# Kernel optimization log

Measured on AMD Instinct MI355X. Metric: run time of the kernel, lower is better.

## Reference

```python
import jax, jax.numpy as jnp
import numpy as np

ALPHA = 0.044194173824159216  # 1/sqrt(512)
EPS = 1e-6
C, G, HW = 512, 32, 4096


def setup_inputs() -> dict:
    key = jax.random.key(0)
    ks = jax.random.split(key, 10)
    s = 1.0 / np.sqrt(C)
    return {
        "x": jax.random.normal(ks[0], (8, C, 64, 64), dtype=jnp.float32),
        "gamma": jnp.ones((C,), jnp.float32),
        "beta": jnp.zeros((C,), jnp.float32),
        "wq": jax.random.uniform(ks[1], (C, C), jnp.float32, -s, s),
        "bq": jax.random.uniform(ks[2], (C,), jnp.float32, -s, s),
        "wk": jax.random.uniform(ks[3], (C, C), jnp.float32, -s, s),
        "bk": jax.random.uniform(ks[4], (C,), jnp.float32, -s, s),
        "wv": jax.random.uniform(ks[5], (C, C), jnp.float32, -s, s),
        "bv": jax.random.uniform(ks[6], (C,), jnp.float32, -s, s),
        "wo": jax.random.uniform(ks[7], (C, C), jnp.float32, -s, s),
        "bo": jax.random.uniform(ks[8], (C,), jnp.float32, -s, s),
    }


def _group_norm(x, gamma, beta):
    B = x.shape[0]
    xg = x.reshape(B, G, C // G, 64, 64)
    mu = jnp.mean(xg, axis=(2, 3, 4), keepdims=True)
    var = jnp.var(xg, axis=(2, 3, 4), keepdims=True)
    xn = ((xg - mu) / jnp.sqrt(var + EPS)).reshape(B, C, 64, 64)
    return xn * gamma[None, :, None, None] + beta[None, :, None, None]


def reference(x, gamma, beta, wq, bq, wk, bk, wv, bv, wo, bo):
    B = x.shape[0]
    res = x
    h = _group_norm(x, gamma, beta)
    # [B, HW, C]
    h = h.reshape(B, C, HW).transpose(0, 2, 1)
    q = h @ wq.T + bq
    k = h @ wk.T + bk
    v = h @ wv.T + bv
    # scores [B, HW, HW]
    scores = ALPHA * jnp.einsum("bnc,bmc->bnm", q, k)
    attn = jax.nn.softmax(scores, axis=2)
    o = jnp.einsum("bnm,bmc->bnc", attn, v)
    o = o @ wo.T + bo
    o = o.transpose(0, 2, 1).reshape(B, C, 64, 64)
    return o + res
```

## Files before the change

kernel.cpp:

```cpp
#include <hip/hip_runtime.h>
#include <hip/hip_bf16.h>

typedef __attribute__((ext_vector_type(8))) short short8;
typedef __attribute__((ext_vector_type(4))) float f32x4;

#define ALPHA 0.044194173824159216f

#define GLO(p) (const __attribute__((address_space(1))) void*)(p)
#define LDSP(p) (__attribute__((address_space(3))) void*)(p)

__device__ __forceinline__ unsigned short f2bf(float f) {
    union { float f; unsigned int u; } c; c.f = f;
    unsigned int u = c.u;
    return (unsigned short)((u + 0x7FFFu + ((u >> 16) & 1u)) >> 16);
}

__device__ __forceinline__ float bf2f(unsigned short s) {
    union { unsigned int u; float f; } c; c.u = ((unsigned int)s) << 16;
    return c.f;
}

__global__ __launch_bounds__(256) void gn_stats(const float* __restrict__ x,
                                                float* __restrict__ stats) {
    int blk = blockIdx.x;
    const float4* src = (const float4*)(x + (size_t)blk * 65536);
    float s = 0.f, sq = 0.f;
    for (int i = threadIdx.x; i < 16384; i += 256) {
        float4 v = src[i];
        s  += v.x + v.y + v.z + v.w;
        sq += v.x*v.x + v.y*v.y + v.z*v.z + v.w*v.w;
    }
    for (int off = 32; off; off >>= 1) {
        s  += __shfl_down(s, off);
        sq += __shfl_down(sq, off);
    }
    __shared__ float ss[4], ssq[4];
    int wid = threadIdx.x >> 6;
    if ((threadIdx.x & 63) == 0) { ss[wid] = s; ssq[wid] = sq; }
    __syncthreads();
    if (threadIdx.x == 0) {
        float S = ss[0]+ss[1]+ss[2]+ss[3], Q = ssq[0]+ssq[1]+ssq[2]+ssq[3];
        float mu = S * (1.f/65536.f);
        float var = Q * (1.f/65536.f) - mu*mu;
        stats[blk] = mu;
        stats[256 + blk] = rsqrtf(var + 1e-6f);
    }
}

__global__ __launch_bounds__(256) void wcvt(const float* __restrict__ s,
                                            unsigned short* __restrict__ d) {
    int i = blockIdx.x * 1024 + threadIdx.x * 4;
    float4 v = *(const float4*)(s + i);
    ushort4 o = make_ushort4(f2bf(v.x), f2bf(v.y), f2bf(v.z), f2bf(v.w));
    *(ushort4*)(d + i) = o;
}

__global__ __launch_bounds__(256) void zero_l(float* __restrict__ l) {
    ((float4*)l)[blockIdx.x * 256 + threadIdx.x] = make_float4(0.f, 0.f, 0.f, 0.f);
}

__global__ __launch_bounds__(256) void recip(float* __restrict__ l) {
    int i = blockIdx.x * 256 + threadIdx.x;
    float4 v = ((const float4*)l)[i];
    ((float4*)l)[i] = make_float4(1.f / v.x, 1.f / v.y, 1.f / v.z, 1.f / v.w);
}

__global__ __launch_bounds__(256) void gn_apply(const float* __restrict__ x,
                                                const float* __restrict__ stats,
                                                const float* __restrict__ gamma,
                                                const float* __restrict__ beta,
                                                unsigned short* __restrict__ h) {
    __shared__ unsigned short t[64][72];
    int b = blockIdx.z, c0 = blockIdx.y * 64, hw0 = blockIdx.x * 64;
    int tid = threadIdx.x;
#pragma unroll
    for (int rep = 0; rep < 4; ++rep) {
        int lin = rep * 256 + tid;
        int row = lin >> 4;
        int c4  = lin & 15;
        int c   = c0 + row;
        const float4* src = (const float4*)(x + ((size_t)(b*512 + c) << 12) + hw0);
        float4 v = src[c4];
        int sidx = b*32 + (c >> 4);
        float mu = stats[sidx], rs = stats[256 + sidx];
        float ga = gamma[c] * rs, be = beta[c] - mu * ga;
        t[c4*4+0][row] = f2bf(v.x * ga + be);
        t[c4*4+1][row] = f2bf(v.y * ga + be);
        t[c4*4+2][row] = f2bf(v.z * ga + be);
        t[c4*4+3][row] = f2bf(v.w * ga + be);
    }
    __syncthreads();
#pragma unroll
    for (int rep = 0; rep < 2; ++rep) {
        int lin = rep * 256 + tid;
        int row = lin >> 3;
        int u8  = lin & 7;
        unsigned short* dst = h + (((size_t)(b*4096 + hw0 + row)) << 9) + c0 + u8*8;
        *(short8*)dst = *(const short8*)&t[row][u8*8];
    }
}

__global__ __launch_bounds__(256, 2) void gemm_bt(const unsigned short* __restrict__ A,
                                                  int lda, long aZs,
                                                  const unsigned short* __restrict__ B,
                                                  int ldb, long bZs,
                                                  const float* __restrict__ bias,
                                                  const float* __restrict__ resid,
                                                  const float* __restrict__ lvec,
                                                  void* __restrict__ out,
                                                  long ldo, long oZs,
                                                  int K, int mode, float scale) {
    __shared__ unsigned short As[128][72], Bs[128][72];
    int z = blockIdx.z;
    A += (size_t)z * aZs;
    B += (size_t)z * bZs;
    unsigned short* outu = (unsigned short*)out + (size_t)z * oZs;
    int m0 = blockIdx.y * 128, n0 = blockIdx.x * 128;
    int tid = threadIdx.x, w = tid >> 6, l = tid & 63;
    int lr = l & 15, lq = l >> 4, lk = lq * 8;
    int rbase = (w >> 1) * 64, cbase = (w & 1) * 64;
    f32x4 acc[4][4] = {};
    for (int k0 = 0; k0 < K; k0 += 64) {
        __syncthreads();
#pragma unroll
        for (int p = 0; p < 4; ++p) {
            int lin = p * 256 + tid;
            int r = lin >> 3, qq = lin & 7;
            *(short8*)&As[r][qq*8] = *(const short8*)(A + (size_t)(m0 + r)*lda + k0 + qq*8);
            *(short8*)&Bs[r][qq*8] = *(const short8*)(B + (size_t)(n0 + r)*ldb + k0 + qq*8);
        }
        __syncthreads();
        short8 af[4][2], bfv[4][2];
#pragma unroll
        for (int i = 0; i < 4; ++i)
#pragma unroll
            for (int ks = 0; ks < 2; ++ks) {
                af[i][ks]  = *(const short8*)&As[rbase + i*16 + lr][ks*32 + lk];
                bfv[i][ks] = *(const short8*)&Bs[cbase + i*16 + lr][ks*32 + lk];
            }
#pragma unroll
        for (int ks = 0; ks < 2; ++ks)
#pragma unroll
            for (int i = 0; i < 4; ++i)
#pragma unroll
                for (int j = 0; j < 4; ++j)
                    acc[i][j] = __builtin_amdgcn_mfma_f32_16x16x32_bf16(af[i][ks], bfv[j][ks], acc[i][j], 0, 0, 0);
    }
    int lq4 = lq * 4;
    if (mode == 2) {
        float rlv[4];
#pragma unroll
        for (int j = 0; j < 4; ++j) rlv[j] = lvec[n0 + cbase + j*16 + lr];
        float* outf = (float*)out;
#pragma unroll
        for (int i = 0; i < 4; ++i) {
            int rowg = m0 + rbase + i*16 + lq4;
            float4 bq4 = *(const float4*)(bias + rowg);
            float bb[4] = {bq4.x, bq4.y, bq4.z, bq4.w};
            size_t ad[16];
            float lres[16];
#pragma unroll
            for (int j = 0; j < 4; ++j) {
                int colg = n0 + cbase + j*16 + lr;
                size_t base = ((size_t)(colg >> 12)) * 2097152 + (size_t)(colg & 4095);
#pragma unroll
                for (int r = 0; r < 4; ++r) {
                    ad[j*4+r] = base + (size_t)(rowg + r) * 4096;
                    lres[j*4+r] = resid[ad[j*4+r]];
                }
            }
#pragma unroll
            for (int j = 0; j < 4; ++j)
#pragma unroll
                for (int r = 0; r < 4; ++r)
                    outf[ad[j*4+r]] = acc[i][j][r] * rlv[j] + bb[r] + lres[j*4+r];
        }
        return;
    }
#pragma unroll
    for (int i = 0; i < 4; ++i) {
        int rowg = m0 + rbase + i*16 + lq4;
#pragma unroll
        for (int j = 0; j < 4; ++j) {
            int colg = n0 + cbase + j*16 + lr;
#pragma unroll
            for (int r = 0; r < 4; ++r) {
                float v = acc[i][j][r];
                int rr = rowg + r;
                if (mode == 0) {
                    outu[(size_t)rr * ldo + colg] = f2bf((v + bias[colg]) * scale);
                } else {
                    outu[(size_t)rr * ldo + colg] = f2bf(v + bias[rr]);
                }
            }
        }
    }
}

__global__ __launch_bounds__(256, 2) void qk2(const unsigned short* __restrict__ A,
                                              const unsigned short* __restrict__ Wq,
                                              const unsigned short* __restrict__ Wk,
                                              const float* __restrict__ biasq,
                                              const float* __restrict__ biask,
                                              unsigned short* __restrict__ qo,
                                              unsigned short* __restrict__ ko) {
    __shared__ unsigned short As[128][72], Bq[128][72], Bk[128][72];
    int m0 = blockIdx.y * 128, n0 = blockIdx.x * 128;
    int tid = threadIdx.x, w = tid >> 6, l = tid & 63;
    int lr = l & 15, lq = l >> 4, lk = lq * 8;
    int rbase = (w >> 1) * 64, cbase = (w & 1) * 64;
    f32x4 aq[4][4] = {}, ak[4][4] = {};
    for (int k0 = 0; k0 < 512; k0 += 64) {
        __syncthreads();
#pragma unroll
        for (int p = 0; p < 4; ++p) {
            int lin = p * 256 + tid;
            int r = lin >> 3, qq = lin & 7;
            *(short8*)&As[r][qq*8] = *(const short8*)(A  + (size_t)(m0 + r)*512 + k0 + qq*8);
            *(short8*)&Bq[r][qq*8] = *(const short8*)(Wq + (size_t)(n0 + r)*512 + k0 + qq*8);
            *(short8*)&Bk[r][qq*8] = *(const short8*)(Wk + (size_t)(n0 + r)*512 + k0 + qq*8);
        }
        __syncthreads();
#pragma unroll
        for (int ks = 0; ks < 2; ++ks) {
            short8 af[4], bfq[4], bfk[4];
#pragma unroll
            for (int i = 0; i < 4; ++i) {
                af[i]  = *(const short8*)&As[rbase + i*16 + lr][ks*32 + lk];
                bfq[i] = *(const short8*)&Bq[cbase + i*16 + lr][ks*32 + lk];
                bfk[i] = *(const short8*)&Bk[cbase + i*16 + lr][ks*32 + lk];
            }
#pragma unroll
            for (int i = 0; i < 4; ++i)
#pragma unroll
                for (int j = 0; j < 4; ++j) {
                    aq[i][j] = __builtin_amdgcn_mfma_f32_16x16x32_bf16(af[i], bfq[j], aq[i][j], 0, 0, 0);
                    ak[i][j] = __builtin_amdgcn_mfma_f32_16x16x32_bf16(af[i], bfk[j], ak[i][j], 0, 0, 0);
                }
        }
    }
    int lq4 = lq * 4;
#pragma unroll
    for (int i = 0; i < 4; ++i) {
        int rowg = m0 + rbase + i*16 + lq4;
#pragma unroll
        for (int j = 0; j < 4; ++j) {
            int colg = n0 + cbase + j*16 + lr;
            float bqv = biasq[colg], bkv = biask[colg];
#pragma unroll
            for (int r = 0; r < 4; ++r) {
                qo[(size_t)(rowg + r) * 512 + colg] = f2bf((aq[i][j][r] + bqv) * ALPHA);
                ko[(size_t)(rowg + r) * 512 + colg] = f2bf(ak[i][j][r] + bkv);
            }
        }
    }
}

__device__ __forceinline__ void mm8_core(const unsigned short* __restrict__ A, int lda,
                                         const unsigned short* __restrict__ B, int ldb,
                                         int T,
                                         unsigned short (*As)[256][64],
                                         unsigned short (*Bs)[256][64],
                                         f32x4 acc[8][4]) {
    int tid = threadIdx.x, w = tid >> 6, l = tid & 63;
    int wr = w >> 2, wc = w & 3;
    int lr = l & 15, lq = l >> 4;
    int rsub = l >> 3, colp = ((l & 7) ^ rsub) << 3;
    int sw = (lr & 7) << 4;
    int aw = w * 8;

#define SG_A(buf, t_) { \
    const unsigned short* ap = A + (size_t)(t_) * 64; \
    __builtin_amdgcn_global_load_lds(GLO(ap + (size_t)(aw + rsub) * lda + colp),        LDSP(&As[buf][aw][0]), 16, 0, 0); \
    __builtin_amdgcn_global_load_lds(GLO(ap + (size_t)(64 + aw + rsub) * lda + colp),   LDSP(&As[buf][64 + aw][0]), 16, 0, 0); \
    __builtin_amdgcn_global_load_lds(GLO(ap + (size_t)(128 + aw + rsub) * lda + colp),  LDSP(&As[buf][128 + aw][0]), 16, 0, 0); \
    __builtin_amdgcn_global_load_lds(GLO(ap + (size_t)(192 + aw + rsub) * lda + colp),  LDSP(&As[buf][192 + aw][0]), 16, 0, 0); }
#define SG_B(buf, t_, h_) { \
    const unsigned short* bp = B + (size_t)(t_) * 64; int rb = (h_) * 128 + aw; \
    __builtin_amdgcn_global_load_lds(GLO(bp + (size_t)(rb + rsub) * ldb + colp),       LDSP(&Bs[buf][rb][0]), 16, 0, 0); \
    __builtin_amdgcn_global_load_lds(GLO(bp + (size_t)(rb + 64 + rsub) * ldb + colp),  LDSP(&Bs[buf][rb + 64][0]), 16, 0, 0); }
#define RD_B() { \
    const char* bsb = (const char*)Bs[cur]; \
    _Pragma("unroll") for (int nj = 0; nj < 4; ++nj) \
    _Pragma("unroll") for (int ks = 0; ks < 2; ++ks) { \
        int row = wc * 64 + nj * 16 + lr; \
        bf[nj][ks] = *(const short8*)(bsb + (((row << 7) + (ks << 6) + (lq << 4)) ^ sw)); } }
#define RD_A(p_) { \
    const char* asb = (const char*)As[cur]; \
    _Pragma("unroll") for (int i = 0; i < 2; ++i) \
    _Pragma("unroll") for (int ks = 0; ks < 2; ++ks) { \
        int row = wr * 128 + ((p_) * 2 + i) * 16 + lr; \
        af[i][ks] = *(const short8*)(asb + (((row << 7) + (ks << 6) + (lq << 4)) ^ sw)); } }
#define MM(p_) { \
    _Pragma("unroll") for (int ks = 0; ks < 2; ++ks) \
    _Pragma("unroll") for (int i = 0; i < 2; ++i) \
    _Pragma("unroll") for (int nj = 0; nj < 4; ++nj) \
        acc[(p_) * 2 + i][nj] = __builtin_amdgcn_mfma_f32_16x16x32_bf16(af[i][ks], bf[nj][ks], acc[(p_) * 2 + i][nj], 0, 0, 0); }
#define LGKM0 { asm volatile("s_waitcnt lgkmcnt(0)" ::: "memory"); __builtin_amdgcn_sched_barrier(0); }
#define VMC4 { asm volatile("s_waitcnt vmcnt(4)" ::: "memory"); __builtin_amdgcn_sched_barrier(0); }
#define VMC0 { asm volatile("s_waitcnt vmcnt(0)" ::: "memory"); __builtin_amdgcn_sched_barrier(0); }
#define BAR __builtin_amdgcn_s_barrier()

    SG_A(0, 0); SG_B(0, 0, 0); SG_B(0, 0, 1);
    if (T > 1) { SG_B(1, 1, 0); SG_B(1, 1, 1); VMC4; } else { VMC0; }
    BAR;
    for (int t = 0; t < T; ++t) {
        int cur = t & 1, nxt = cur ^ 1;
        short8 bf[4][2], af[2][2];
        RD_B(); RD_A(0);
        if (t + 1 < T) SG_A(nxt, t + 1);
        BAR; LGKM0;
        __builtin_amdgcn_s_setprio(1); MM(0); __builtin_amdgcn_s_setprio(0);
        BAR;
        RD_A(1);
        if (t + 2 < T) SG_B(cur, t + 2, 0);
        BAR; LGKM0;
        __builtin_amdgcn_s_setprio(1); MM(1); __builtin_amdgcn_s_setprio(0);
        BAR;
        RD_A(2);
        if (t + 2 < T) SG_B(cur, t + 2, 1);
        BAR; LGKM0;
        __builtin_amdgcn_s_setprio(1); MM(2); __builtin_amdgcn_s_setprio(0);
        BAR;
        RD_A(3);
        if (t + 2 < T) { VMC4; } else { VMC0; }
        BAR; LGKM0;
        __builtin_amdgcn_s_setprio(1); MM(3); __builtin_amdgcn_s_setprio(0);
        BAR;
    }
#undef SG_A
#undef SG_B
#undef RD_B
#undef RD_A
#undef MM
#undef LGKM0
#undef VMC4
#undef VMC0
#undef BAR
}

__global__ __launch_bounds__(512, 2) void s8(const unsigned short* __restrict__ q,
                                             const unsigned short* __restrict__ k,
                                             float* __restrict__ lout,
                                             unsigned short* __restrict__ P0,
                                             unsigned short* __restrict__ P1,
                                             int nwg) {
    __shared__ unsigned short As[2][256][64], Bs[2][256][64];
    int wk = (int)(blockIdx.x & 7) * (nwg >> 3) + (int)(blockIdx.x >> 3);
    int z = wk >> 8, rem = wk & 255;
    int m0 = (rem >> 4) << 8, n0 = (rem & 15) << 8;
    const unsigned short* A = k + (size_t)z * 2097152 + (size_t)m0 * 512;
    const unsigned short* B = q + (size_t)z * 2097152 + (size_t)n0 * 512;
    f32x4 acc[8][4] = {};
    mm8_core(A, 512, B, 512, 8, As, Bs, acc);
    unsigned short* Pz = (z < 2) ? P0 + (size_t)z * 16777216
                                 : P1 + (size_t)(z - 2) * 16777216;
    float* lz = lout + z * 4096;
    int tid = threadIdx.x, w = tid >> 6, l = tid & 63;
    int wr = w >> 2, wc = w & 3, lr = l & 15, lq = l >> 4, lq4 = lq * 4;
    int jb = m0 + wr * 128;
    int ib = n0 + wc * 64;
#pragma unroll
    for (int nj = 0; nj < 4; ++nj) {
        int i = ib + nj * 16 + lr;
        unsigned short* prow = Pz + (size_t)i * 4096 + jb + lq4;
        float rs = 0.f;
#pragma unroll
        for (int mi = 0; mi < 8; ++mi) {
            float e0 = __expf(acc[mi][nj][0]);
            float e1 = __expf(acc[mi][nj][1]);
            float e2 = __expf(acc[mi][nj][2]);
            float e3 = __expf(acc[mi][nj][3]);
            rs += (e0 + e1) + (e2 + e3);
            ushort4 pk = make_ushort4(f2bf(e0), f2bf(e1), f2bf(e2), f2bf(e3));
            *(ushort4*)(prow + mi * 16) = pk;
        }
        rs += __shfl_xor(rs, 16);
        rs += __shfl_xor(rs, 32);
        if (lq == 0) atomicAdd(&lz[i], rs);
    }
}

__global__ __launch_bounds__(512, 2) void pv8(const unsigned short* __restrict__ P0,
                                              const unsigned short* __restrict__ P1,
                                              const unsigned short* __restrict__ vt,
                                              unsigned short* __restrict__ part0,
                                              unsigned short* __restrict__ part1,
                                              int zofs, int nwg) {
    __shared__ unsigned short As[2][256][64], Bs[2][256][64];
    int wk = (int)(blockIdx.x & 7) * (nwg >> 3) + (int)(blockIdx.x >> 3);
    int half = nwg >> 1;
    int s = (wk >= half) ? 1 : 0;
    int rem = wk - s * half;
    int z = rem >> 5, t2 = rem & 31;
    int m0 = (t2 >> 1) << 8, n0 = (t2 & 1) << 8;
    const unsigned short* Pz = (z < 2) ? P0 + (size_t)z * 16777216
                                       : P1 + (size_t)(z - 2) * 16777216;
    const unsigned short* A = Pz + (size_t)m0 * 4096 + (size_t)s * 2048;
    const unsigned short* B = vt + (size_t)n0 * 32768 + (size_t)(zofs + z) * 4096 + (size_t)s * 2048;
    f32x4 acc[8][4] = {};
    mm8_core(A, 4096, B, 32768, 32, As, Bs, acc);
    unsigned short* pp = (s ? part1 : part0) + (size_t)z * 2097152 + (size_t)m0 * 512 + n0;
    int tid = threadIdx.x, w = tid >> 6, l = tid & 63;
    int wr = w >> 2, wc = w & 3, lr = l & 15, lq4 = (l >> 4) * 4;
#pragma unroll
    for (int mi = 0; mi < 8; ++mi)
#pragma unroll
        for (int nj = 0; nj < 4; ++nj)
#pragma unroll
            for (int r = 0; r < 4; ++r)
                pp[(size_t)(wr * 128 + mi * 16 + lq4 + r) * 512 + wc * 64 + nj * 16 + lr] = f2bf(acc[mi][nj][r]);
}

__global__ __launch_bounds__(256) void addcvt(const unsigned short* __restrict__ p0,
                                              const unsigned short* __restrict__ p1,
                                              unsigned short* __restrict__ o) {
    size_t i = ((size_t)blockIdx.x * 256 + threadIdx.x) * 8;
    short8 a = *(const short8*)(p0 + i), b = *(const short8*)(p1 + i);
    short8 r;
#pragma unroll
    for (int j = 0; j < 8; ++j)
        r[j] = (short)f2bf(bf2f((unsigned short)a[j]) + bf2f((unsigned short)b[j]));
    *(short8*)(o + i) = r;
}

extern "C" void kernel_launch(void* const* d_in, const int* in_sizes, int n_in,
                              void* d_out, int out_size, void* d_ws, size_t ws_size,
                              hipStream_t stream) {
    const float* x     = (const float*)d_in[0];
    const float* gamma = (const float*)d_in[1];
    const float* beta  = (const float*)d_in[2];
    const float* wq = (const float*)d_in[3];  const float* bq = (const float*)d_in[4];
    const float* wk = (const float*)d_in[5];  const float* bk = (const float*)d_in[6];
    const float* wv = (const float*)d_in[7];  const float* bv = (const float*)d_in[8];
    const float* wo = (const float*)d_in[9];  const float* bo = (const float*)d_in[10];

    char* wsp = (char*)d_ws;
    float* stats        = (float*)wsp;
    unsigned short* wqb = (unsigned short*)(wsp + 2048);
    unsigned short* wkb = wqb + 262144;
    unsigned short* wvb = wkb + 262144;
    unsigned short* wob = wvb + 262144;
    unsigned short* h   = wob + 262144;
    unsigned short* qb  = h  + 16777216;
    unsigned short* kb  = qb + 16777216;
    unsigned short* vtb = kb + 16777216;
    float* lbuf         = (float*)(vtb + 16777216);
    unsigned short* Pw  = (unsigned short*)(lbuf + 32768);
    unsigned short* Pd  = (unsigned short*)d_out;
    unsigned short* ob  = h;

    const bool mid = ws_size >= 204000000ull;

    gn_stats<<<256, 256, 0, stream>>>(x, stats);
    wcvt<<<256, 256, 0, stream>>>(wq, wqb);
    wcvt<<<256, 256, 0, stream>>>(wk, wkb);
    wcvt<<<256, 256, 0, stream>>>(wv, wvb);
    wcvt<<<256, 256, 0, stream>>>(wo, wob);
    gn_apply<<<dim3(64, 8, 8), 256, 0, stream>>>(x, stats, gamma, beta, h);
    zero_l<<<32, 256, 0, stream>>>(lbuf);

    qk2<<<dim3(4, 256), 256, 0, stream>>>(h, wqb, wkb, bq, bk, qb, kb);
    gemm_bt<<<dim3(256, 4), 256, 0, stream>>>(wvb, 512, 0, h, 512, 0, bv, nullptr, nullptr,
                                              vtb, 32768, 0, 512, 1, 1.0f);

    const long QS = (long)4096 * 512;
    if (mid) {
        for (int c = 0; c < 2; ++c) {
            size_t z0 = (size_t)c * 4;
            s8<<<1024, 512, 0, stream>>>(qb + z0 * QS, kb + z0 * QS,
                                         lbuf + z0 * 4096, Pd, Pw, 1024);
            pv8<<<256, 512, 0, stream>>>(Pd, Pw, vtb,
                                         qb + z0 * QS, kb + z0 * QS, (int)z0, 256);
            addcvt<<<4096, 256, 0, stream>>>(qb + z0 * QS, kb + z0 * QS, ob + z0 * QS);
        }
    } else {
        for (int c = 0; c < 4; ++c) {
            size_t z0 = (size_t)c * 2;
            s8<<<512, 512, 0, stream>>>(qb + z0 * QS, kb + z0 * QS,
                                        lbuf + z0 * 4096, Pd, Pd, 512);
            pv8<<<128, 512, 0, stream>>>(Pd, Pd, vtb,
                                         qb + z0 * QS, kb + z0 * QS, (int)z0, 128);
            addcvt<<<2048, 256, 0, stream>>>(qb + z0 * QS, kb + z0 * QS, ob + z0 * QS);
        }
    }
    recip<<<32, 256, 0, stream>>>(lbuf);
    gemm_bt<<<dim3(256, 4), 256, 0, stream>>>(wob, 512, 0, ob, 512, 0, bo, x, lbuf,
                                              d_out, 0, 0, 512, 2, 1.0f);
}
```

Before: 681.5 us.

## Fuse split-K partial add into output GEMM and replace atomics with partial sums

Removes the addcvt pass that summed the two split-K halves of the attention output, and instead has the output-projection GEMM accumulate over both partial buffers in two K passes. Row-sum atomics in s8 are replaced by per-block LDS reductions written to a partial buffer in the freed h region, and the recip kernel sums those partials. This drops the zero_l launch and a full read/write pass over the attention output, but doubles the K loop in the final GEMM and adds a 16-way partial reduction.

New measurement: 674.3 us. About the same (-1.1%).

```diff
diff --git a/kernel.cpp b/kernel.cpp
--- a/kernel.cpp
+++ b/kernel.cpp
@@ -55,14 +55,16 @@
     *(ushort4*)(d + i) = o;
 }
 
-__global__ __launch_bounds__(256) void zero_l(float* __restrict__ l) {
-    ((float4*)l)[blockIdx.x * 256 + threadIdx.x] = make_float4(0.f, 0.f, 0.f, 0.f);
-}
-
-__global__ __launch_bounds__(256) void recip(float* __restrict__ l) {
+__global__ __launch_bounds__(256) void recip(const float* __restrict__ lpart,
+                                             float* __restrict__ l) {
     int i = blockIdx.x * 256 + threadIdx.x;
-    float4 v = ((const float4*)l)[i];
-    ((float4*)l)[i] = make_float4(1.f / v.x, 1.f / v.y, 1.f / v.z, 1.f / v.w);
+    float4 s = make_float4(0.f, 0.f, 0.f, 0.f);
+#pragma unroll
+    for (int jt = 0; jt < 16; ++jt) {
+        float4 v = ((const float4*)(lpart + (size_t)jt * 32768))[i];
+        s.x += v.x; s.y += v.y; s.z += v.z; s.w += v.w;
+    }
+    ((float4*)l)[i] = make_float4(1.f/s.x, 1.f/s.y, 1.f/s.z, 1.f/s.w);
 }
 
 __global__ __launch_bounds__(256) void gn_apply(const float* __restrict__ x,
@@ -104,6 +106,7 @@
                                                   int lda, long aZs,
                                                   const unsigned short* __restrict__ B,
                                                   int ldb, long bZs,
+                                                  const unsigned short* __restrict__ B2,
                                                   const float* __restrict__ bias,
                                                   const float* __restrict__ resid,
                                                   const float* __restrict__ lvec,
@@ -120,31 +123,36 @@
     int lr = l & 15, lq = l >> 4, lk = lq * 8;
     int rbase = (w >> 1) * 64, cbase = (w & 1) * 64;
     f32x4 acc[4][4] = {};
-    for (int k0 = 0; k0 < K; k0 += 64) {
-        __syncthreads();
-#pragma unroll
-        for (int p = 0; p < 4; ++p) {
-            int lin = p * 256 + tid;
-            int r = lin >> 3, qq = lin & 7;
-            *(short8*)&As[r][qq*8] = *(const short8*)(A + (size_t)(m0 + r)*lda + k0 + qq*8);
-            *(short8*)&Bs[r][qq*8] = *(const short8*)(B + (size_t)(n0 + r)*ldb + k0 + qq*8);
-        }
-        __syncthreads();
-        short8 af[4][2], bfv[4][2];
-#pragma unroll
-        for (int i = 0; i < 4; ++i)
-#pragma unroll
-            for (int ks = 0; ks < 2; ++ks) {
-                af[i][ks]  = *(const short8*)&As[rbase + i*16 + lr][ks*32 + lk];
-                bfv[i][ks] = *(const short8*)&Bs[cbase + i*16 + lr][ks*32 + lk];
+    int passes = (mode == 2) ? 2 : 1;
+    const unsigned short* Bsrc = B;
+    for (int ps = 0; ps < passes; ++ps) {
+        if (ps) Bsrc = B2;
+        for (int k0 = 0; k0 < K; k0 += 64) {
+            __syncthreads();
+#pragma unroll
+            for (int p = 0; p < 4; ++p) {
+                int lin = p * 256 + tid;
+                int r = lin >> 3, qq = lin & 7;
+                *(short8*)&As[r][qq*8] = *(const short8*)(A + (size_t)(m0 + r)*lda + k0 + qq*8);
+                *(short8*)&Bs[r][qq*8] = *(const short8*)(Bsrc + (size_t)(n0 + r)*ldb + k0 + qq*8);
             }
-#pragma unroll
-        for (int ks = 0; ks < 2; ++ks)
+            __syncthreads();
+            short8 af[4][2], bfv[4][2];
 #pragma unroll
             for (int i = 0; i < 4; ++i)
 #pragma unroll
-                for (int j = 0; j < 4; ++j)
-                    acc[i][j] = __builtin_amdgcn_mfma_f32_16x16x32_bf16(af[i][ks], bfv[j][ks], acc[i][j], 0, 0, 0);
+                for (int ks = 0; ks < 2; ++ks) {
+                    af[i][ks]  = *(const short8*)&As[rbase + i*16 + lr][ks*32 + lk];
+                    bfv[i][ks] = *(const short8*)&Bs[cbase + i*16 + lr][ks*32 + lk];
+                }
+#pragma unroll
+            for (int ks = 0; ks < 2; ++ks)
+#pragma unroll
+                for (int i = 0; i < 4; ++i)
+#pragma unroll
+                    for (int j = 0; j < 4; ++j)
+                        acc[i][j] = __builtin_amdgcn_mfma_f32_16x16x32_bf16(af[i][ks], bfv[j][ks], acc[i][j], 0, 0, 0);
+        }
     }
     int lq4 = lq * 4;
     if (mode == 2) {
@@ -184,15 +192,8 @@
         for (int j = 0; j < 4; ++j) {
             int colg = n0 + cbase + j*16 + lr;
 #pragma unroll
-            for (int r = 0; r < 4; ++r) {
-                float v = acc[i][j][r];
-                int rr = rowg + r;
-                if (mode == 0) {
-                    outu[(size_t)rr * ldo + colg] = f2bf((v + bias[colg]) * scale);
-                } else {
-                    outu[(size_t)rr * ldo + colg] = f2bf(v + bias[rr]);
-                }
-            }
+            for (int r = 0; r < 4; ++r)
+                outu[(size_t)(rowg + r) * ldo + colg] = f2bf(acc[i][j][r] + bias[rowg + r]);
         }
     }
 }
@@ -341,10 +342,10 @@
 
 __global__ __launch_bounds__(512, 2) void s8(const unsigned short* __restrict__ q,
                                              const unsigned short* __restrict__ k,
-                                             float* __restrict__ lout,
+                                             float* __restrict__ lpart,
                                              unsigned short* __restrict__ P0,
                                              unsigned short* __restrict__ P1,
-                                             int nwg) {
+                                             int zofs, int nwg) {
     __shared__ unsigned short As[2][256][64], Bs[2][256][64];
     int wk = (int)(blockIdx.x & 7) * (nwg >> 3) + (int)(blockIdx.x >> 3);
     int z = wk >> 8, rem = wk & 255;
@@ -355,15 +356,14 @@
     mm8_core(A, 512, B, 512, 8, As, Bs, acc);
     unsigned short* Pz = (z < 2) ? P0 + (size_t)z * 16777216
                                  : P1 + (size_t)(z - 2) * 16777216;
-    float* lz = lout + z * 4096;
     int tid = threadIdx.x, w = tid >> 6, l = tid & 63;
     int wr = w >> 2, wc = w & 3, lr = l & 15, lq = l >> 4, lq4 = lq * 4;
     int jb = m0 + wr * 128;
-    int ib = n0 + wc * 64;
+    float* lsum = (float*)As;
 #pragma unroll
     for (int nj = 0; nj < 4; ++nj) {
-        int i = ib + nj * 16 + lr;
-        unsigned short* prow = Pz + (size_t)i * 4096 + jb + lq4;
+        int iloc = wc * 64 + nj * 16 + lr;
+        unsigned short* prow = Pz + (size_t)(n0 + iloc) * 4096 + jb + lq4;
         float rs = 0.f;
 #pragma unroll
         for (int mi = 0; mi < 8; ++mi) {
@@ -377,7 +377,12 @@
         }
         rs += __shfl_xor(rs, 16);
         rs += __shfl_xor(rs, 32);
-        if (lq == 0) atomicAdd(&lz[i], rs);
+        if (lq == 0) lsum[wr * 256 + iloc] = rs;
+    }
+    __syncthreads();
+    if (tid < 256) {
+        float v = lsum[tid] + lsum[256 + tid];
+        lpart[(size_t)(m0 >> 8) * 32768 + (size_t)(zofs + z) * 4096 + n0 + tid] = v;
     }
 }
 
@@ -412,18 +417,6 @@
                 pp[(size_t)(wr * 128 + mi * 16 + lq4 + r) * 512 + wc * 64 + nj * 16 + lr] = f2bf(acc[mi][nj][r]);
 }
 
-__global__ __launch_bounds__(256) void addcvt(const unsigned short* __restrict__ p0,
-                                              const unsigned short* __restrict__ p1,
-                                              unsigned short* __restrict__ o) {
-    size_t i = ((size_t)blockIdx.x * 256 + threadIdx.x) * 8;
-    short8 a = *(const short8*)(p0 + i), b = *(const short8*)(p1 + i);
-    short8 r;
-#pragma unroll
-    for (int j = 0; j < 8; ++j)
-        r[j] = (short)f2bf(bf2f((unsigned short)a[j]) + bf2f((unsigned short)b[j]));
-    *(short8*)(o + i) = r;
-}
-
 extern "C" void kernel_launch(void* const* d_in, const int* in_sizes, int n_in,
                               void* d_out, int out_size, void* d_ws, size_t ws_size,
                               hipStream_t stream) {
@@ -448,7 +441,7 @@
     float* lbuf         = (float*)(vtb + 16777216);
     unsigned short* Pw  = (unsigned short*)(lbuf + 32768);
     unsigned short* Pd  = (unsigned short*)d_out;
-    unsigned short* ob  = h;
+    float* lpart        = (float*)h;
 
     const bool mid = ws_size >= 204000000ull;
 
@@ -458,10 +451,9 @@
     wcvt<<<256, 256, 0, stream>>>(wv, wvb);
     wcvt<<<256, 256, 0, stream>>>(wo, wob);
     gn_apply<<<dim3(64, 8, 8), 256, 0, stream>>>(x, stats, gamma, beta, h);
-    zero_l<<<32, 256, 0, stream>>>(lbuf);
 
     qk2<<<dim3(4, 256), 256, 0, stream>>>(h, wqb, wkb, bq, bk, qb, kb);
-    gemm_bt<<<dim3(256, 4), 256, 0, stream>>>(wvb, 512, 0, h, 512, 0, bv, nullptr, nullptr,
+    gemm_bt<<<dim3(256, 4), 256, 0, stream>>>(wvb, 512, 0, h, 512, 0, nullptr, bv, nullptr, nullptr,
                                               vtb, 32768, 0, 512, 1, 1.0f);
 
     const long QS = (long)4096 * 512;
@@ -469,22 +461,20 @@
         for (int c = 0; c < 2; ++c) {
             size_t z0 = (size_t)c * 4;
             s8<<<1024, 512, 0, stream>>>(qb + z0 * QS, kb + z0 * QS,
-                                         lbuf + z0 * 4096, Pd, Pw, 1024);
+                                         lpart, Pd, Pw, (int)z0, 1024);
             pv8<<<256, 512, 0, stream>>>(Pd, Pw, vtb,
                                          qb + z0 * QS, kb + z0 * QS, (int)z0, 256);
-            addcvt<<<4096, 256, 0, stream>>>(qb + z0 * QS, kb + z0 * QS, ob + z0 * QS);
         }
     } else {
         for (int c = 0; c < 4; ++c) {
             size_t z0 = (size_t)c * 2;
             s8<<<512, 512, 0, stream>>>(qb + z0 * QS, kb + z0 * QS,
-                                        lbuf + z0 * 4096, Pd, Pd, 512);
+                                        lpart, Pd, Pd, (int)z0, 512);
             pv8<<<128, 512, 0, stream>>>(Pd, Pd, vtb,
                                          qb + z0 * QS, kb + z0 * QS, (int)z0, 128);
-            addcvt<<<2048, 256, 0, stream>>>(qb + z0 * QS, kb + z0 * QS, ob + z0 * QS);
-        }
-    }
-    recip<<<32, 256, 0, stream>>>(lbuf);
-    gemm_bt<<<dim3(256, 4), 256, 0, stream>>>(wob, 512, 0, ob, 512, 0, bo, x, lbuf,
+        }
+    }
+    recip<<<32, 256, 0, stream>>>(lpart, lbuf);
+    gemm_bt<<<dim3(256, 4), 256, 0, stream>>>(wob, 512, 0, qb, 512, 0, kb, bo, x, lbuf,
                                               d_out, 0, 0, 512, 2, 1.0f);
 }
```
